# Kernel tuning notes

Hardware: AMD Instinct MI355X
Metric: run time of the kernel (lower is better)

The kernel has to match this reference:

```python
import jax, jax.numpy as jnp
import numpy as np

QMAX = 7.0      # symmetric int4 magnitude
GROUP = 64      # weight quant group size along input dim
RANK = 32       # SVD low-rank correction rank
EPS = 1e-8


def quantize_act(x):
    # per-token symmetric int4 fake-quant: scale = max|x| / 7 over feature dim
    s = jnp.maximum(jnp.max(jnp.abs(x), axis=-1, keepdims=True) / QMAX, EPS)
    q = jnp.clip(jnp.round(x / s), -8.0, 7.0)
    return q * s


def quantize_weight(w):
    # per-output-channel, per-group (GROUP along input dim) symmetric int4 fake-quant
    O, D = w.shape
    wg = w.reshape(O, D // GROUP, GROUP)
    s = jnp.maximum(jnp.max(jnp.abs(wg), axis=-1, keepdims=True) / QMAX, EPS)
    q = jnp.clip(jnp.round(wg / s), -8.0, 7.0)
    return (q * s).reshape(O, D)


def setup_inputs() -> dict:
    key = jax.random.key(0)
    k0, k1, k2, k3 = jax.random.split(key, 4)
    dim_in, dim_out2 = 3072, 24576
    x = jax.random.normal(k0, (1, 4096, dim_in), dtype=jnp.float32)
    w_res = jax.random.normal(k1, (dim_out2, dim_in), dtype=jnp.float32) * 0.02
    lora_down = jax.random.normal(k2, (RANK, dim_in), dtype=jnp.float32) * 0.02
    lora_up = jax.random.normal(k3, (dim_out2, RANK), dtype=jnp.float32) * 0.02
    return {"x": x, "w_res": w_res, "lora_down": lora_down, "lora_up": lora_up}


def reference(x, w_res, lora_down, lora_up):
    # SVDQW4A4Linear: quantized residual matmul + fp low-rank correction
    xq = quantize_act(x)                        # [B, S, D]
    wq = quantize_weight(w_res)                 # [O, D]
    out = jnp.einsum('bsd,od->bso', xq, wq)
    out = out + jnp.einsum('bsr,or->bso', jnp.einsum('bsd,rd->bsr', x, lora_down), lora_up)
    # GEGLU epilogue: chunk(2, dim=-1), x * gelu(gate)  (torch F.gelu = exact erf)
    h, gate = jnp.split(out, 2, axis=-1)
    return h * jax.nn.gelu(gate, approximate=False)
```

## Files before the change

### kernel.cpp

```cpp
#include <hip/hip_runtime.h>
#include <hip/hip_bf16.h>
#include <math.h>

typedef __bf16 bf16_t;
typedef __bf16 bf16x4 __attribute__((ext_vector_type(4)));
typedef __bf16 bf16x8 __attribute__((ext_vector_type(8)));
typedef float  f32x4  __attribute__((ext_vector_type(4)));

#define DIN   3072
#define NOUT  24576
#define HALF  12288
#define MTOK  4096
#define BK    64
#define NT    48

#define GLD16(gp, lp) \
    __builtin_amdgcn_global_load_lds((const __attribute__((address_space(1))) void*)(gp), \
                                     (__attribute__((address_space(3))) void*)(lp), 16, 0, 0)

#define BAR()    __builtin_amdgcn_s_barrier()
#define LGKM0()  asm volatile("s_waitcnt lgkmcnt(0)" ::: "memory")
#define WAITV(N) asm volatile("s_waitcnt vmcnt(" #N ")" ::: "memory")
#define PRIO1()  __builtin_amdgcn_s_setprio(1)
#define PRIO0()  __builtin_amdgcn_s_setprio(0)

__global__ __launch_bounds__(256) void k_quant_x(const float* __restrict__ x,
                                                 bf16_t* __restrict__ xq) {
    int m = blockIdx.x;
    int t = threadIdx.x;
    const float4* row = reinterpret_cast<const float4*>(x + (size_t)m * DIN);
    float4 v[3];
    float vm = 0.f;
#pragma unroll
    for (int i = 0; i < 3; ++i) {
        v[i] = row[t + i * 256];
        vm = fmaxf(vm, fmaxf(fmaxf(fabsf(v[i].x), fabsf(v[i].y)),
                             fmaxf(fabsf(v[i].z), fabsf(v[i].w))));
    }
#pragma unroll
    for (int d = 1; d < 64; d <<= 1) vm = fmaxf(vm, __shfl_xor(vm, d));
    __shared__ float sm[4];
    if ((t & 63) == 0) sm[t >> 6] = vm;
    __syncthreads();
    vm = fmaxf(fmaxf(sm[0], sm[1]), fmaxf(sm[2], sm[3]));
    float s = fmaxf(vm * (1.f / 7.f), 1e-8f);
    float inv = 1.f / s;
    bf16x4* orow = reinterpret_cast<bf16x4*>(xq + (size_t)m * DIN);
#pragma unroll
    for (int i = 0; i < 3; ++i) {
        bf16x4 o;
        o[0] = (bf16_t)(fminf(fmaxf(rintf(v[i].x * inv), -8.f), 7.f) * s);
        o[1] = (bf16_t)(fminf(fmaxf(rintf(v[i].y * inv), -8.f), 7.f) * s);
        o[2] = (bf16_t)(fminf(fmaxf(rintf(v[i].z * inv), -8.f), 7.f) * s);
        o[3] = (bf16_t)(fminf(fmaxf(rintf(v[i].w * inv), -8.f), 7.f) * s);
        orow[t + i * 256] = o;
    }
}

__global__ __launch_bounds__(256) void k_quant_w(const float* __restrict__ w,
                                                 bf16_t* __restrict__ wq) {
    size_t idx = (size_t)blockIdx.x * 256 + threadIdx.x;
    float4 v = reinterpret_cast<const float4*>(w)[idx];
    float vm = fmaxf(fmaxf(fabsf(v.x), fabsf(v.y)), fmaxf(fabsf(v.z), fabsf(v.w)));
    vm = fmaxf(vm, __shfl_xor(vm, 1));
    vm = fmaxf(vm, __shfl_xor(vm, 2));
    vm = fmaxf(vm, __shfl_xor(vm, 4));
    vm = fmaxf(vm, __shfl_xor(vm, 8));
    float s = fmaxf(vm * (1.f / 7.f), 1e-8f);
    float inv = 1.f / s;
    bf16x4 o;
    o[0] = (bf16_t)(fminf(fmaxf(rintf(v.x * inv), -8.f), 7.f) * s);
    o[1] = (bf16_t)(fminf(fmaxf(rintf(v.y * inv), -8.f), 7.f) * s);
    o[2] = (bf16_t)(fminf(fmaxf(rintf(v.z * inv), -8.f), 7.f) * s);
    o[3] = (bf16_t)(fminf(fmaxf(rintf(v.w * inv), -8.f), 7.f) * s);
    reinterpret_cast<bf16x4*>(wq)[idx] = o;
}

__global__ __launch_bounds__(256) void k_lora_t(const float* __restrict__ x,
                                                const float* __restrict__ ld,
                                                bf16_t* __restrict__ T) {
    int r = threadIdx.x & 31;
    int m = blockIdx.x * 8 + (threadIdx.x >> 5);
    const float4* xr = reinterpret_cast<const float4*>(x + (size_t)m * DIN);
    const float4* lr = reinterpret_cast<const float4*>(ld + (size_t)r * DIN);
    float acc = 0.f;
#pragma unroll 4
    for (int i = 0; i < DIN / 4; ++i) {
        float4 a = xr[i], b = lr[i];
        acc += a.x * b.x + a.y * b.y + a.z * b.z + a.w * b.w;
    }
    T[(size_t)m * 32 + r] = (bf16_t)acc;
}

__global__ __launch_bounds__(256) void k_cvt_lu(const float* __restrict__ lu,
                                                bf16_t* __restrict__ lub) {
    size_t idx = (size_t)blockIdx.x * 256 + threadIdx.x;
    float4 v = reinterpret_cast<const float4*>(lu)[idx];
    bf16x4 o;
    o[0] = (bf16_t)v.x; o[1] = (bf16_t)v.y; o[2] = (bf16_t)v.z; o[3] = (bf16_t)v.w;
    reinterpret_cast<bf16x4*>(lub)[idx] = o;
}


#define STAGE_UNIT(gbase, sbase)                                              \
    do {                                                                      \
        _Pragma("unroll")                                                     \
        for (int _r = 0; _r < 2; ++_r) {                                      \
            int _c = _r * 512 + tid;                                          \
            int _row = _c >> 3;                                               \
            int _gc = ((_c & 7) ^ (_row & 7)) * 8;                            \
            GLD16((gbase) + (size_t)_row * DIN + _gc, (sbase) + _c * 16);     \
        }                                                                     \
    } while (0)

#define LOAD_A(mh)                                                            \
    _Pragma("unroll")                                                         \
    for (int _i = 0; _i < 4; ++_i) {                                          \
        _Pragma("unroll")                                                     \
        for (int _ks = 0; _ks < 2; ++_ks) {                                   \
            int _ra = (mh) * 128 + wr * 64 + _i * 16 + l15;                   \
            int _c16 = _ks * 4 + lhi;                                         \
            a[_i][_ks] = *(const bf16x8*)(sAc + _ra * 128 + ((_c16 ^ lk) << 4)); \
        }                                                                     \
    }

#define LOAD_B(nh)                                                            \
    _Pragma("unroll")                                                         \
    for (int _j = 0; _j < 2; ++_j) {                                          \
        _Pragma("unroll")                                                     \
        for (int _ks = 0; _ks < 2; ++_ks) {                                   \
            int _rb = wc * 64 + ((nh) * 2 + _j) * 16 + l15;                   \
            int _c16 = _ks * 4 + lhi;                                         \
            b[(nh) * 2 + _j][_ks] = *(const bf16x8*)(sBc + _rb * 128 + ((_c16 ^ lk) << 4)); \
        }                                                                     \
    }

#define MFMA_Q(mh, nh)                                                        \
    _Pragma("unroll")                                                         \
    for (int _i = 0; _i < 4; ++_i) {                                          \
        _Pragma("unroll")                                                     \
        for (int _j = 0; _j < 2; ++_j) {                                      \
            _Pragma("unroll")                                                 \
            for (int _ks = 0; _ks < 2; ++_ks) {                               \
                acc[(mh) * 4 + _i][(nh) * 2 + _j] =                           \
                    __builtin_amdgcn_mfma_f32_16x16x32_bf16(                  \
                        a[_i][_ks], b[(nh) * 2 + _j][_ks],                    \
                        acc[(mh) * 4 + _i][(nh) * 2 + _j], 0, 0, 0);          \
            }                                                                 \
        }                                                                     \
    }

__global__ __launch_bounds__(512, 2) void k_gemm(const bf16_t* __restrict__ xq,
                                                 const bf16_t* __restrict__ wq,
                                                 const bf16_t* __restrict__ T,
                                                 const bf16_t* __restrict__ lub,
                                                 float* __restrict__ out) {
    __shared__ __align__(16) char smem[131072];

    const int tid = threadIdx.x, lane = tid & 63, w = tid >> 6;
    const int half = w >> 2;
    const int wr = (w >> 1) & 1, wc = w & 1;
    const int l15 = lane & 15, lhi = lane >> 4, lk = lane & 7;

    const int nwg = gridDim.x;
    const int cpx = nwg >> 3;
    const int swz = ((int)blockIdx.x & 7) * cpx + ((int)blockIdx.x >> 3);
    const int mt = swz & 15, nt = swz >> 4;
    const int m0 = mt * 256, c0 = nt * 128;

    f32x4 acc[8][4];
#pragma unroll
    for (int i = 0; i < 8; ++i)
#pragma unroll
        for (int j = 0; j < 4; ++j) acc[i][j] = (f32x4){0.f, 0.f, 0.f, 0.f};

    const bf16_t* gA = xq + (size_t)m0 * DIN;
    const bf16_t* gH = wq + (size_t)c0 * DIN;
    const bf16_t* gG = wq + (size_t)(c0 + HALF) * DIN;

    STAGE_UNIT(gA, smem);
    STAGE_UNIT(gH, smem + 32768);
    STAGE_UNIT(gG, smem + 49152);
    STAGE_UNIT(gA + (size_t)128 * DIN, smem + 16384);
    WAITV(2);
    BAR();

    int cur = 0;
    for (int t = 0; t < NT; ++t) {
        const int kc = (t + 1 < NT) ? (t + 1) * BK : t * BK;
        char* sw = smem + (cur ^ 1) * 65536;
        const char* sAc = smem + cur * 65536;
        const char* sBc = sAc + 32768 + half * 16384;

        bf16x8 a[4][2], b[4][2];

        LOAD_A(0); LOAD_B(0);
        STAGE_UNIT(gA + kc, sw);
        BAR(); LGKM0(); PRIO1(); MFMA_Q(0, 0); PRIO0(); BAR();
        LOAD_B(1);
        STAGE_UNIT(gH + kc, sw + 32768);
        BAR(); LGKM0(); PRIO1(); MFMA_Q(0, 1); PRIO0(); WAITV(4); BAR();
        LOAD_A(1);
        STAGE_UNIT(gG + kc, sw + 49152);
        BAR(); LGKM0(); PRIO1(); MFMA_Q(1, 0); PRIO0(); BAR();
        STAGE_UNIT(gA + (size_t)128 * DIN + kc, sw + 16384);
        BAR(); LGKM0(); PRIO1(); MFMA_Q(1, 1); PRIO0(); WAITV(2); BAR();

        cur ^= 1;
    }

    {
        bf16x8 tf[8];
#pragma unroll
        for (int m = 0; m < 8; ++m) {
            int row = m0 + (m >> 2) * 128 + wr * 64 + (m & 3) * 16 + l15;
            tf[m] = *reinterpret_cast<const bf16x8*>(T + (size_t)row * 32 + lhi * 8);
        }
#pragma unroll
        for (int n = 0; n < 4; ++n) {
            int ocol = c0 + half * HALF + wc * 64 + n * 16 + l15;
            bf16x8 lu = *reinterpret_cast<const bf16x8*>(lub + (size_t)ocol * 32 + lhi * 8);
#pragma unroll
            for (int m = 0; m < 8; ++m)
                acc[m][n] = __builtin_amdgcn_mfma_f32_16x16x32_bf16(tf[m], lu, acc[m][n], 0, 0, 0);
        }
    }

    WAITV(0);
    __syncthreads();
    float* exch = (float*)smem;
    if (half) {
#pragma unroll
        for (int m = 0; m < 8; ++m)
#pragma unroll
            for (int n = 0; n < 4; ++n) {
                int col = wc * 64 + n * 16 + l15;
#pragma unroll
                for (int r = 0; r < 4; ++r) {
                    int row = (m >> 2) * 128 + wr * 64 + (m & 3) * 16 + lhi * 4 + r;
                    float g = acc[m][n][r];
                    float gl = 0.5f * g * (1.0f + erff(g * 0.70710678118654752f));
                    exch[row * 128 + (col ^ (((row >> 2) & 3) << 4))] = gl;
                }
            }
    }
    __syncthreads();
    if (!half) {
#pragma unroll
        for (int m = 0; m < 8; ++m)
#pragma unroll
            for (int n = 0; n < 4; ++n) {
                int col = wc * 64 + n * 16 + l15;
#pragma unroll
                for (int r = 0; r < 4; ++r) {
                    int row = (m >> 2) * 128 + wr * 64 + (m & 3) * 16 + lhi * 4 + r;
                    float gl = exch[row * 128 + (col ^ (((row >> 2) & 3) << 4))];
                    out[(size_t)(m0 + row) * HALF + c0 + col] = acc[m][n][r] * gl;
                }
            }
    }
}

extern "C" void kernel_launch(void* const* d_in, const int* in_sizes, int n_in,
                              void* d_out, int out_size, void* d_ws, size_t ws_size,
                              hipStream_t stream) {
    const float* x  = (const float*)d_in[0];
    const float* wr = (const float*)d_in[1];
    const float* ld = (const float*)d_in[2];
    const float* lu = (const float*)d_in[3];
    float* out = (float*)d_out;

    bf16_t* xq  = (bf16_t*)d_ws;
    bf16_t* wq  = xq + (size_t)MTOK * DIN;
    bf16_t* T   = wq + (size_t)NOUT * DIN;
    bf16_t* lub = T  + (size_t)MTOK * 32;

    k_quant_x<<<MTOK, 256, 0, stream>>>(x, xq);
    k_quant_w<<<(NOUT * (DIN / 4)) / 256, 256, 0, stream>>>(wr, wq);
    k_lora_t<<<MTOK / 8, 256, 0, stream>>>(x, ld, T);
    k_cvt_lu<<<(NOUT * 32 / 4) / 256, 256, 0, stream>>>(lu, lub);
    k_gemm<<<(MTOK / 256) * (HALF / 128), 512, 0, stream>>>(xq, wq, T, lub, out);
}
```

Before: 891.0 us.

## Prefetch next-tile A fragments and precompute per-thread global staging pointers

The GEMM main loop is restructured so that the first A fragment for the next K tile is read from LDS at the end of each iteration. It overlaps with the tail of the current MFMA work instead of sitting at the start of the next iteration. Staging addresses are now computed once per thread as eight incrementing global pointers, replacing the per-call row and swizzle arithmetic. The B fragments are split into separate register arrays, and extra vmcnt waits are added between phases. The change costs more live registers at 2 waves per SIMD and tighter wait and barrier ordering.

```diff
diff --git a/kernel.cpp b/kernel.cpp
--- a/kernel.cpp
+++ b/kernel.cpp
@@ -102,40 +102,29 @@
 }
 
 
-#define STAGE_UNIT(gbase, sbase)                                              \
-    do {                                                                      \
-        _Pragma("unroll")                                                     \
-        for (int _r = 0; _r < 2; ++_r) {                                      \
-            int _c = _r * 512 + tid;                                          \
-            int _row = _c >> 3;                                               \
-            int _gc = ((_c & 7) ^ (_row & 7)) * 8;                            \
-            GLD16((gbase) + (size_t)_row * DIN + _gc, (sbase) + _c * 16);     \
-        }                                                                     \
-    } while (0)
-
-#define LOAD_A(mh)                                                            \
+#define LOADA(dst, mh, base)                                                  \
     _Pragma("unroll")                                                         \
     for (int _i = 0; _i < 4; ++_i) {                                          \
         _Pragma("unroll")                                                     \
         for (int _ks = 0; _ks < 2; ++_ks) {                                   \
             int _ra = (mh) * 128 + wr * 64 + _i * 16 + l15;                   \
-            int _c16 = _ks * 4 + lhi;                                         \
-            a[_i][_ks] = *(const bf16x8*)(sAc + _ra * 128 + ((_c16 ^ lk) << 4)); \
+            dst[_i][_ks] = *(const bf16x8*)((base) + _ra * 128 +              \
+                                            (((_ks * 4 + lhi) ^ lk) << 4));   \
         }                                                                     \
     }
 
-#define LOAD_B(nh)                                                            \
+#define LOADB(dst, nh, base)                                                  \
     _Pragma("unroll")                                                         \
     for (int _j = 0; _j < 2; ++_j) {                                          \
         _Pragma("unroll")                                                     \
         for (int _ks = 0; _ks < 2; ++_ks) {                                   \
             int _rb = wc * 64 + ((nh) * 2 + _j) * 16 + l15;                   \
-            int _c16 = _ks * 4 + lhi;                                         \
-            b[(nh) * 2 + _j][_ks] = *(const bf16x8*)(sBc + _rb * 128 + ((_c16 ^ lk) << 4)); \
+            dst[_j][_ks] = *(const bf16x8*)((base) + _rb * 128 +              \
+                                            (((_ks * 4 + lhi) ^ lk) << 4));   \
         }                                                                     \
     }
 
-#define MFMA_Q(mh, nh)                                                        \
+#define MFMAQ(mh, nh, A, B)                                                   \
     _Pragma("unroll")                                                         \
     for (int _i = 0; _i < 4; ++_i) {                                          \
         _Pragma("unroll")                                                     \
@@ -144,11 +133,17 @@
             for (int _ks = 0; _ks < 2; ++_ks) {                               \
                 acc[(mh) * 4 + _i][(nh) * 2 + _j] =                           \
                     __builtin_amdgcn_mfma_f32_16x16x32_bf16(                  \
-                        a[_i][_ks], b[(nh) * 2 + _j][_ks],                    \
+                        A[_i][_ks], B[_j][_ks],                               \
                         acc[(mh) * 4 + _i][(nh) * 2 + _j], 0, 0, 0);          \
             }                                                                 \
         }                                                                     \
     }
+
+#define STG(pl, ph, off)                                                      \
+    do {                                                                      \
+        GLD16((pl), swc + (off) + wq4);                                       \
+        GLD16((ph), swc + (off) + wq4 + 8192);                                \
+    } while (0)
 
 __global__ __launch_bounds__(512, 2) void k_gemm(const bf16_t* __restrict__ xq,
                                                  const bf16_t* __restrict__ wq,
@@ -161,6 +156,7 @@
     const int half = w >> 2;
     const int wr = (w >> 1) & 1, wc = w & 1;
     const int l15 = lane & 15, lhi = lane >> 4, lk = lane & 7;
+    const int wq4 = w * 1024;
 
     const int nwg = gridDim.x;
     const int cpx = nwg >> 3;
@@ -174,38 +170,55 @@
 #pragma unroll
         for (int j = 0; j < 4; ++j) acc[i][j] = (f32x4){0.f, 0.f, 0.f, 0.f};
 
-    const bf16_t* gA = xq + (size_t)m0 * DIN;
-    const bf16_t* gH = wq + (size_t)c0 * DIN;
-    const bf16_t* gG = wq + (size_t)(c0 + HALF) * DIN;
-
-    STAGE_UNIT(gA, smem);
-    STAGE_UNIT(gH, smem + 32768);
-    STAGE_UNIT(gG, smem + 49152);
-    STAGE_UNIT(gA + (size_t)128 * DIN, smem + 16384);
+    const int srow = tid >> 3;
+    const int sgc = ((tid & 7) ^ (srow & 7)) * 8;
+    const bf16_t* pA0l = xq + (size_t)(m0 + srow) * DIN + sgc;
+    const bf16_t* pA0h = pA0l + (size_t)64 * DIN;
+    const bf16_t* pA1l = pA0l + (size_t)128 * DIN;
+    const bf16_t* pA1h = pA0l + (size_t)192 * DIN;
+    const bf16_t* pHl  = wq + (size_t)(c0 + srow) * DIN + sgc;
+    const bf16_t* pHh  = pHl + (size_t)64 * DIN;
+    const bf16_t* pGl  = pHl + (size_t)HALF * DIN;
+    const bf16_t* pGh  = pGl + (size_t)64 * DIN;
+
+    bf16x8 aP[4][2], a2[4][2], b0[2][2], b1[2][2];
+
+    {
+        char* swc = (char*)smem;
+        STG(pA0l, pA0h, 0);
+        STG(pHl, pHh, 32768);
+        STG(pGl, pGh, 49152);
+        STG(pA1l, pA1h, 16384);
+    }
+    pA0l += BK; pA0h += BK; pA1l += BK; pA1h += BK;
+    pHl += BK; pHh += BK; pGl += BK; pGh += BK;
     WAITV(2);
     BAR();
+    LOADA(aP, 0, (const char*)smem);
 
     int cur = 0;
     for (int t = 0; t < NT; ++t) {
-        const int kc = (t + 1 < NT) ? (t + 1) * BK : t * BK;
-        char* sw = smem + (cur ^ 1) * 65536;
-        const char* sAc = smem + cur * 65536;
-        const char* sBc = sAc + 32768 + half * 16384;
-
-        bf16x8 a[4][2], b[4][2];
-
-        LOAD_A(0); LOAD_B(0);
-        STAGE_UNIT(gA + kc, sw);
-        BAR(); LGKM0(); PRIO1(); MFMA_Q(0, 0); PRIO0(); BAR();
-        LOAD_B(1);
-        STAGE_UNIT(gH + kc, sw + 32768);
-        BAR(); LGKM0(); PRIO1(); MFMA_Q(0, 1); PRIO0(); WAITV(4); BAR();
-        LOAD_A(1);
-        STAGE_UNIT(gG + kc, sw + 49152);
-        BAR(); LGKM0(); PRIO1(); MFMA_Q(1, 0); PRIO0(); BAR();
-        STAGE_UNIT(gA + (size_t)128 * DIN + kc, sw + 16384);
-        BAR(); LGKM0(); PRIO1(); MFMA_Q(1, 1); PRIO0(); WAITV(2); BAR();
-
+        const char* sAc = (const char*)smem + (cur << 16);
+        const char* sBc = sAc + 32768 + (half << 14);
+        char* swc = (char*)smem + ((cur ^ 1) << 16);
+
+        LOADB(b0, 0, sBc);
+        STG(pA0l, pA0h, 0);
+        BAR(); LGKM0(); PRIO1(); MFMAQ(0, 0, aP, b0); PRIO0(); WAITV(4); BAR();
+        LOADB(b1, 1, sBc);
+        STG(pHl, pHh, 32768);
+        BAR(); LGKM0(); PRIO1(); MFMAQ(0, 1, aP, b1); PRIO0(); WAITV(4); BAR();
+        LOADA(a2, 1, sAc);
+        STG(pGl, pGh, 49152);
+        BAR(); LGKM0(); PRIO1(); MFMAQ(1, 0, a2, b0); PRIO0(); WAITV(4); BAR();
+        STG(pA1l, pA1h, 16384);
+        BAR(); LGKM0(); PRIO1(); MFMAQ(1, 1, a2, b1); PRIO0();
+        LOADA(aP, 0, (const char*)swc);
+        WAITV(2); BAR();
+
+        const int adv = (t + 2 < NT) ? BK : 0;
+        pA0l += adv; pA0h += adv; pA1l += adv; pA1h += adv;
+        pHl += adv; pHh += adv; pGl += adv; pGh += adv;
         cur ^= 1;
     }
 
```

Measured after the change: 882.5 us. About the same (-1.0%).
